# Kernel optimization log

Hardware: AMD Instinct MI355X
Metric: run time of the kernel (lower is better)

Reference implementation:

```python
import jax, jax.numpy as jnp
import numpy as np

B, MAXN, F, H, T, L = 32, 1024, 215, 256, 8, 3
N = B * MAXN            # 32768 global nodes
E = 524288              # total edges, global indices


def setup_inputs() -> dict:
    key = jax.random.key(0)
    ks = jax.random.split(key, 12)
    s = 0.05
    return {
        "node_features": jax.random.normal(ks[0], (B, MAXN, F), dtype=jnp.float32),
        "edge_index": jax.random.randint(ks[1], (2, E), 0, N, dtype=jnp.int32),
        "edge_type": jax.random.randint(ks[2], (E,), 0, T, dtype=jnp.int32),
        # input projection
        "Wp": jax.random.normal(ks[3], (H, F), dtype=jnp.float32) * s,
        "bp": jax.random.normal(ks[4], (H,), dtype=jnp.float32) * s,
        # per-layer, per-edge-type message linears
        "Wm": jax.random.normal(ks[5], (L, T, H, H), dtype=jnp.float32) * s,
        "bm": jax.random.normal(ks[6], (L, T, H), dtype=jnp.float32) * s,
        # per-layer GRUCell params (torch layout: [r|z|n] stacked, 3H rows)
        "Wih": jax.random.normal(ks[7], (L, 3 * H, H), dtype=jnp.float32) * s,
        "Whh": jax.random.normal(ks[8], (L, 3 * H, H), dtype=jnp.float32) * s,
        "bih": jax.random.normal(ks[9], (L, 3 * H), dtype=jnp.float32) * s,
        "bhh": jax.random.normal(ks[10], (L, 3 * H), dtype=jnp.float32) * s,
    }


def _gru_cell(x, h, Wih, Whh, bih, bhh):
    # torch.nn.GRUCell math
    gi = x @ Wih.T + bih            # (N, 3H)
    gh = h @ Whh.T + bhh            # (N, 3H)
    i_r, i_z, i_n = jnp.split(gi, 3, axis=-1)
    h_r, h_z, h_n = jnp.split(gh, 3, axis=-1)
    r = jax.nn.sigmoid(i_r + h_r)
    z = jax.nn.sigmoid(i_z + h_z)
    n = jnp.tanh(i_n + r * h_n)
    return (1.0 - z) * n + z * h


def reference(node_features, edge_index, edge_type, Wp, bp, Wm, bm, Wih, Whh, bih, bhh):
    # flatten batch of graphs into global node array, project to hidden
    h = node_features.reshape(-1, F) @ Wp.T + bp          # (N, H)
    src, dst = edge_index[0], edge_index[1]
    for l in range(L):
        # apply all T type-specific linears to every node once (equivalent to
        # the per-edge-type mask+gather+Linear loop), then gather per edge
        Ht = jnp.einsum('nd,ted->nte', h, Wm[l]) + bm[l]  # (N, T, H)
        msg = Ht[src, edge_type]                           # (E, H) gather
        m = jax.ops.segment_sum(msg, dst, num_segments=N)  # scatter-add (N, H)
        h = _gru_cell(m, h, Wih[l], Whh[l], bih[l], bhh[l])
        # dropout is identity in eval mode
    # readout: full graphs -> sum each graph's node block
    return h.reshape(B, MAXN, H).sum(axis=1)               # (B, H)
```

## Files before the change

### kernel.cpp

```cpp
#include <hip/hip_runtime.h>

#define N_NODES 32768
#define E_EDGES 524288
#define F_IN    215
#define H_DIM   256
#define T_TYPES 8
#define L_LAYERS 3
#define B_GRAPHS 32
#define MAXN_   1024
#define NT_BINS (N_NODES * T_TYPES)

typedef float  f32x4  __attribute__((ext_vector_type(4)));
typedef __bf16 bf16x8 __attribute__((ext_vector_type(8)));

__device__ __forceinline__ unsigned short f2bf(float f) {
  union { float f; unsigned u; } v; v.f = f;
  unsigned r = v.u + 0x7fffu + ((v.u >> 16) & 1u);
  return (unsigned short)(r >> 16);
}
__device__ __forceinline__ float bf2f(unsigned short h) {
  union { unsigned u; float f; } v; v.u = ((unsigned)h) << 16;
  return v.f;
}
__device__ __forceinline__ float bflo(unsigned u) { union { unsigned x; float f; } v; v.x = u << 16; return v.f; }
__device__ __forceinline__ float bfhi(unsigned u) { union { unsigned x; float f; } v; v.x = u & 0xffff0000u; return v.f; }

typedef const __attribute__((address_space(1))) unsigned int* gas_ptr;
typedef __attribute__((address_space(3))) unsigned int* las_ptr;
__device__ __forceinline__ void gload_lds16(const unsigned short* g, unsigned short* l) {
  __builtin_amdgcn_global_load_lds((gas_ptr)g, (las_ptr)l, 16, 0, 0);
}

__device__ __forceinline__ void acc16(float* a, const uint4 v, const uint4 w) {
  a[0]  += bflo(v.x); a[1]  += bfhi(v.x);
  a[2]  += bflo(v.y); a[3]  += bfhi(v.y);
  a[4]  += bflo(v.z); a[5]  += bfhi(v.z);
  a[6]  += bflo(v.w); a[7]  += bfhi(v.w);
  a[8]  += bflo(w.x); a[9]  += bfhi(w.x);
  a[10] += bflo(w.y); a[11] += bfhi(w.y);
  a[12] += bflo(w.z); a[13] += bfhi(w.z);
  a[14] += bflo(w.w); a[15] += bfhi(w.w);
}

static constexpr size_t OFF_BIG     = 0;
static constexpr size_t REL_CURSOR  = 1048576;
static constexpr size_t REL_BSUM    = 2097152;
static constexpr size_t REL_WPPAD   = 33554432;
static constexpr size_t REL_HALT    = 50331648;
static constexpr size_t REL_OFFS    = 100663296;
static constexpr size_t REL_SORTED  = 104857600;
static constexpr size_t OFF_H_B     = 134217728;
static constexpr size_t OFF_M_B     = 150994944;
static constexpr size_t OFF_WMB     = 167772160;
static constexpr size_t OFF_WIH     = 170917888;
static constexpr size_t OFF_WHH     = 172097536;
static constexpr size_t WS_REQUIRED = 173277184;

__global__ void hist_kernel(const int* __restrict__ dst, const int* __restrict__ et,
                            int* __restrict__ cnt) {
  int e = blockIdx.x * 256 + threadIdx.x;
  atomicAdd(&cnt[dst[e] * T_TYPES + et[e]], 1);
}

__global__ __launch_bounds__(1024) void scan1(const int* __restrict__ cnt,
                                              int* __restrict__ offs,
                                              int* __restrict__ bsum) {
  __shared__ int wsum[16];
  const int t = threadIdx.x, lane = t & 63, wid = t >> 6;
  const int idx = blockIdx.x * 1024 + t;
  const int v = cnt[idx];
  int x = v;
  #pragma unroll
  for (int off = 1; off < 64; off <<= 1) {
    int u = __shfl_up(x, off, 64);
    if (lane >= off) x += u;
  }
  if (lane == 63) wsum[wid] = x;
  __syncthreads();
  int wbase = 0;
  for (int i = 0; i < wid; ++i) wbase += wsum[i];
  offs[idx] = wbase + x - v;
  if (t == 1023) bsum[blockIdx.x] = wbase + x;
}

__global__ __launch_bounds__(256) void scan2(int* __restrict__ bsum) {
  __shared__ int wsum[4];
  const int t = threadIdx.x, lane = t & 63, wid = t >> 6;
  const int v = bsum[t];
  int x = v;
  #pragma unroll
  for (int off = 1; off < 64; off <<= 1) {
    int u = __shfl_up(x, off, 64);
    if (lane >= off) x += u;
  }
  if (lane == 63) wsum[wid] = x;
  __syncthreads();
  int wbase = 0;
  for (int i = 0; i < wid; ++i) wbase += wsum[i];
  __syncthreads();
  bsum[t] = wbase + x - v;
}

__global__ __launch_bounds__(1024) void scan3(int* __restrict__ offs,
                                              const int* __restrict__ bsum,
                                              int* __restrict__ cursor) {
  const int idx = blockIdx.x * 1024 + threadIdx.x;
  const int o = offs[idx] + bsum[blockIdx.x];
  offs[idx] = o;
  cursor[idx] = o;
  if (idx == 0) offs[NT_BINS] = E_EDGES;
}

__global__ void reorder_kernel(const int* __restrict__ src, const int* __restrict__ dst,
                               const int* __restrict__ et, int* __restrict__ cursor,
                               unsigned short* __restrict__ sorted) {
  int e = blockIdx.x * 256 + threadIdx.x;
  int key = dst[e] * T_TYPES + et[e];
  int p = atomicAdd(&cursor[key], 1);
  sorted[p] = (unsigned short)src[e];
}

__global__ void cvt_weights(const float* __restrict__ a, const float* __restrict__ b,
                            const float* __restrict__ c,
                            unsigned short* __restrict__ oa, unsigned short* __restrict__ ob,
                            unsigned short* __restrict__ oc,
                            int na, int nb, int nc) {
  int i = blockIdx.x * 256 + threadIdx.x;
  if (i < na) { oa[i] = f2bf(a[i]); return; }
  int j = i - na;
  if (j < nb) { ob[j] = f2bf(b[j]); return; }
  int k = j - nb;
  if (k < nc) oc[k] = f2bf(c[k]);
}

__global__ void pad_cvt(const float* __restrict__ in, unsigned short* __restrict__ out,
                        int rows, int cin) {
  int i = blockIdx.x * 256 + threadIdx.x;
  if (i >= rows * 256) return;
  int r = i >> 8, c = i & 255;
  out[i] = (c < cin) ? f2bf(in[(size_t)r * cin + c]) : (unsigned short)0;
}

__global__ __launch_bounds__(256, 2) void gemm_bt(
    const unsigned short* __restrict__ A,
    const unsigned short* __restrict__ W,
    const float* __restrict__ bias,
    unsigned short* __restrict__ C,
    int M, int K) {
  __shared__ unsigned short As[128 * 32];
  __shared__ unsigned short Bs[128 * 32];
  const int tid = threadIdx.x;
  const int lane = tid & 63;
  const int wv = tid >> 6;
  const int lrow = lane & 15;
  const int lquad = lane >> 4;
  const int bm0 = blockIdx.x * 128;
  const int bn0 = blockIdx.y * 128;
  const int srow = wv * 16 + (lane >> 2);
  const int scol = (lane & 3) * 8;

  f32x4 acc[2][8] = {};

  for (int kt = 0; kt < K; kt += 32) {
    #pragma unroll
    for (int i = 0; i < 2; ++i) {
      const int row = srow + i * 64;
      gload_lds16(A + (size_t)(bm0 + row) * K + kt + scol, &As[row * 32 + scol]);
      gload_lds16(W + (size_t)(bn0 + row) * K + kt + scol, &Bs[row * 32 + scol]);
    }
    __syncthreads();
    bf16x8 af[2], bfr[8];
    #pragma unroll
    for (int mt = 0; mt < 2; ++mt)
      af[mt] = *(const bf16x8*)(&As[(wv * 32 + mt * 16 + lrow) * 32 + lquad * 8]);
    #pragma unroll
    for (int nt = 0; nt < 8; ++nt)
      bfr[nt] = *(const bf16x8*)(&Bs[(nt * 16 + lrow) * 32 + lquad * 8]);
    #pragma unroll
    for (int mt = 0; mt < 2; ++mt)
      #pragma unroll
      for (int nt = 0; nt < 8; ++nt)
        acc[mt][nt] = __builtin_amdgcn_mfma_f32_16x16x32_bf16(af[mt], bfr[nt], acc[mt][nt], 0, 0, 0);
    __syncthreads();
  }

  #pragma unroll
  for (int mt = 0; mt < 2; ++mt) {
    #pragma unroll
    for (int r = 0; r < 4; ++r) {
      const int grow = bm0 + wv * 32 + mt * 16 + lquad * 4 + r;
      #pragma unroll
      for (int nt = 0; nt < 8; ++nt) {
        const int gcol = bn0 + nt * 16 + lrow;
        float v = acc[mt][nt][r] + (bias ? bias[gcol] : 0.f);
        C[(size_t)grow * M + gcol] = f2bf(v);
      }
    }
  }
}

__global__ __launch_bounds__(512, 4) void msg_gemm(
    const int* __restrict__ offs, const unsigned short* __restrict__ sorted,
    const unsigned short* __restrict__ hb, const unsigned short* __restrict__ Wt_l,
    const float* __restrict__ bm_l, unsigned short* __restrict__ m) {
  constexpr int CH = 2568;
  __shared__ unsigned short Ss[8 * CH];
  __shared__ unsigned short Bs[2][256 * 32];
  __shared__ unsigned short idxS[2048];
  __shared__ int offsS[516];
  const int tid = threadIdx.x;
  const int lane = tid & 63;
  const int wv = tid >> 6;
  const int lrow = lane & 15;
  const int lquad = lane >> 4;
  const int wrow = wv & 3;
  const int wcol = wv >> 2;
  const int bm0 = blockIdx.x * 64;
  const int gg = wv * 4 + lquad;
  const int brow = tid >> 2;
  const int bcol = (tid & 3) * 8;

  const int gseg0 = offs[bm0 * 8];
  const int gseg1 = offs[bm0 * 8 + 512];
  const int seg = gseg1 - gseg0;
  for (int i = tid; i < 513; i += 512) offsS[i] = offs[bm0 * 8 + i];
  const int segc = seg < 2048 ? seg : 2048;
  for (int i = tid; i < segc; i += 512) idxS[i] = sorted[gseg0 + i];
  const bool useLds = (seg <= 2048);
  const unsigned short* ip = useLds ? (const unsigned short*)idxS : (sorted + gseg0);
  __syncthreads();

  f32x4 acc[8] = {};
  int buf = 0;

  for (int t = 0; t < T_TYPES; ++t) {
    #pragma unroll
    for (int step = 0; step < 2; ++step) {
      const int dloc = gg + step * 32;
      const int beg = offsS[dloc * 8 + t] - gseg0;
      const int end = offsS[dloc * 8 + t + 1] - gseg0;
      float a[16];
      #pragma unroll
      for (int j = 0; j < 16; ++j) a[j] = 0.f;
      int e = beg;
      if (e + 2 <= end) {
        int s0 = ip[e], s1 = ip[e + 1];
        const unsigned short* h0 = hb + (size_t)s0 * H_DIM + lrow * 16;
        const unsigned short* h1 = hb + (size_t)s1 * H_DIM + lrow * 16;
        uint4 pv0 = *(const uint4*)h0, pw0 = *(const uint4*)(h0 + 8);
        uint4 pv1 = *(const uint4*)h1, pw1 = *(const uint4*)(h1 + 8);
        e += 2;
        for (; e + 2 <= end; e += 2) {
          const int n0 = ip[e], n1 = ip[e + 1];
          const unsigned short* g0 = hb + (size_t)n0 * H_DIM + lrow * 16;
          const unsigned short* g1 = hb + (size_t)n1 * H_DIM + lrow * 16;
          const uint4 nv0 = *(const uint4*)g0, nw0 = *(const uint4*)(g0 + 8);
          const uint4 nv1 = *(const uint4*)g1, nw1 = *(const uint4*)(g1 + 8);
          acc16(a, pv0, pw0);
          acc16(a, pv1, pw1);
          pv0 = nv0; pw0 = nw0; pv1 = nv1; pw1 = nw1;
        }
        acc16(a, pv0, pw0);
        acc16(a, pv1, pw1);
      }
      if (e < end) {
        const int s0 = ip[e];
        const unsigned short* h0 = hb + (size_t)s0 * H_DIM + lrow * 16;
        acc16(a, *(const uint4*)h0, *(const uint4*)(h0 + 8));
      }
      union { unsigned short us[16]; uint4 q[2]; } ob;
      #pragma unroll
      for (int j = 0; j < 16; ++j) ob.us[j] = f2bf(a[j]);
      uint4* p = (uint4*)&Ss[(lrow >> 1) * CH + dloc * 40 + (lrow & 1) * 16];
      p[0] = ob.q[0];
      p[1] = ob.q[1];
    }
    const unsigned short* Wt = Wt_l + (size_t)t * 65536;
    gload_lds16(Wt + (size_t)brow * 256 + bcol, &Bs[buf][brow * 32 + bcol]);
    gload_lds16(Wt + (size_t)(brow + 128) * 256 + bcol, &Bs[buf][(brow + 128) * 32 + bcol]);
    __syncthreads();
    for (int kc = 0; kc < 8; ++kc) {
      if (kc < 7) {
        gload_lds16(Wt + (size_t)brow * 256 + (kc + 1) * 32 + bcol,
                    &Bs[buf ^ 1][brow * 32 + bcol]);
        gload_lds16(Wt + (size_t)(brow + 128) * 256 + (kc + 1) * 32 + bcol,
                    &Bs[buf ^ 1][(brow + 128) * 32 + bcol]);
      }
      const bf16x8 af = *(const bf16x8*)(&Ss[kc * CH + (wrow * 16 + lrow) * 40 + lquad * 8]);
      #pragma unroll
      for (int nt = 0; nt < 8; ++nt) {
        const bf16x8 b = *(const bf16x8*)(&Bs[buf][((wcol * 8 + nt) * 16 + lrow) * 32 + lquad * 8]);
        acc[nt] = __builtin_amdgcn_mfma_f32_16x16x32_bf16(af, b, acc[nt], 0, 0, 0);
      }
      buf ^= 1;
      __syncthreads();
    }
  }

  float cnt[4][8];
  #pragma unroll
  for (int r = 0; r < 4; ++r) {
    const int dl = wrow * 16 + lquad * 4 + r;
    #pragma unroll
    for (int t = 0; t < 8; ++t)
      cnt[r][t] = (float)(offsS[dl * 8 + t + 1] - offsS[dl * 8 + t]);
  }
  #pragma unroll
  for (int nt = 0; nt < 8; ++nt) {
    const int gcol = wcol * 128 + nt * 16 + lrow;
    float bmv[8];
    #pragma unroll
    for (int t = 0; t < 8; ++t) bmv[t] = bm_l[t * H_DIM + gcol];
    #pragma unroll
    for (int r = 0; r < 4; ++r) {
      const int grow = bm0 + wrow * 16 + lquad * 4 + r;
      float v = acc[nt][r];
      #pragma unroll
      for (int t = 0; t < 8; ++t) v += cnt[r][t] * bmv[t];
      m[(size_t)grow * H_DIM + gcol] = f2bf(v);
    }
  }
}

__global__ __launch_bounds__(256, 3) void gru_fused(
    const unsigned short* __restrict__ mB,
    const unsigned short* __restrict__ hin,
    const unsigned short* __restrict__ wih_l,
    const unsigned short* __restrict__ whh_l,
    const float* __restrict__ bih_l,
    const float* __restrict__ bhh_l,
    unsigned short* __restrict__ hout) {
  __shared__ unsigned short Am[64 * 32];
  __shared__ unsigned short Ah[64 * 32];
  const int tid = threadIdx.x;
  const int lane = tid & 63;
  const int wv = tid >> 6;
  const int lrow = lane & 15;
  const int lquad = lane >> 4;
  const int n0 = blockIdx.x * 64;
  const int c0 = blockIdx.y * 64;
  const int arow = tid >> 2;
  const int scol = (tid & 3) * 8;

  f32x4 acc[6][4] = {};

  for (int kt = 0; kt < 256; kt += 32) {
    __syncthreads();
    gload_lds16(mB  + (size_t)(n0 + arow) * 256 + kt + scol, &Am[arow * 32 + scol]);
    gload_lds16(hin + (size_t)(n0 + arow) * 256 + kt + scol, &Ah[arow * 32 + scol]);
    __syncthreads();
    const int wr = c0 + wv * 16 + lrow;
    bf16x8 bfr[6];
    #pragma unroll
    for (int g = 0; g < 3; ++g) {
      bfr[g]     = *(const bf16x8*)(wih_l + (size_t)(g * 256 + wr) * 256 + kt + lquad * 8);
      bfr[g + 3] = *(const bf16x8*)(whh_l + (size_t)(g * 256 + wr) * 256 + kt + lquad * 8);
    }
    #pragma unroll
    for (int mt = 0; mt < 4; ++mt) {
      const bf16x8 am = *(const bf16x8*)(&Am[(mt * 16 + lrow) * 32 + lquad * 8]);
      const bf16x8 ah = *(const bf16x8*)(&Ah[(mt * 16 + lrow) * 32 + lquad * 8]);
      #pragma unroll
      for (int g = 0; g < 6; ++g)
        acc[g][mt] = __builtin_amdgcn_mfma_f32_16x16x32_bf16(g < 3 ? am : ah, bfr[g], acc[g][mt], 0, 0, 0);
    }
  }

  const int c = c0 + wv * 16 + lrow;
  const float b_ir = bih_l[c], b_iz = bih_l[256 + c], b_in = bih_l[512 + c];
  const float b_hr = bhh_l[c], b_hz = bhh_l[256 + c], b_hn = bhh_l[512 + c];
  #pragma unroll
  for (int mt = 0; mt < 4; ++mt) {
    #pragma unroll
    for (int r = 0; r < 4; ++r) {
      const int node = n0 + mt * 16 + lquad * 4 + r;
      const float i_r = acc[0][mt][r] + b_ir;
      const float i_z = acc[1][mt][r] + b_iz;
      const float i_n = acc[2][mt][r] + b_in;
      const float h_r = acc[3][mt][r] + b_hr;
      const float h_z = acc[4][mt][r] + b_hz;
      const float h_n = acc[5][mt][r] + b_hn;
      const float rr = 1.f / (1.f + __expf(-(i_r + h_r)));
      const float zz = 1.f / (1.f + __expf(-(i_z + h_z)));
      const float nn = tanhf(i_n + rr * h_n);
      const float hp = bf2f(hin[(size_t)node * 256 + c]);
      hout[(size_t)node * 256 + c] = f2bf((1.f - zz) * nn + zz * hp);
    }
  }
}

__global__ __launch_bounds__(256) void readout_partial(const unsigned short* __restrict__ hb,
                                                       float* __restrict__ part) {
  const int b = blockIdx.x >> 3;
  const int ch = blockIdx.x & 7;
  const int c = threadIdx.x;
  const unsigned short* base = hb + ((size_t)b * MAXN_ + ch * 128) * H_DIM + c;
  float s = 0.f;
  #pragma unroll 4
  for (int i = 0; i < 128; ++i) s += bf2f(base[(size_t)i * H_DIM]);
  part[(size_t)blockIdx.x * H_DIM + c] = s;
}

__global__ __launch_bounds__(256) void readout_final(const float* __restrict__ part,
                                                     float* __restrict__ out) {
  const int b = blockIdx.x;
  const int c = threadIdx.x;
  float s = 0.f;
  #pragma unroll
  for (int i = 0; i < 8; ++i) s += part[((size_t)b * 8 + i) * H_DIM + c];
  out[b * H_DIM + c] = s;
}

extern "C" void kernel_launch(void* const* d_in, const int* in_sizes, int n_in,
                              void* d_out, int out_size, void* d_ws, size_t ws_size,
                              hipStream_t stream) {
  if (ws_size < WS_REQUIRED) return;

  const float* X   = (const float*)d_in[0];
  const int*   ei  = (const int*)d_in[1];
  const int*   et  = (const int*)d_in[2];
  const float* Wp  = (const float*)d_in[3];
  const float* bp  = (const float*)d_in[4];
  const float* Wm  = (const float*)d_in[5];
  const float* bm  = (const float*)d_in[6];
  const float* Wih = (const float*)d_in[7];
  const float* Whh = (const float*)d_in[8];
  const float* bih = (const float*)d_in[9];
  const float* bhh = (const float*)d_in[10];
  float* out = (float*)d_out;
  char* ws = (char*)d_ws;

  int*            counts = (int*)(ws + OFF_BIG);
  int*            cursor = (int*)(ws + OFF_BIG + REL_CURSOR);
  int*            bsum   = (int*)(ws + OFF_BIG + REL_BSUM);
  unsigned short* xpad   = (unsigned short*)(ws + OFF_BIG);
  unsigned short* wppad  = (unsigned short*)(ws + OFF_BIG + REL_WPPAD);
  unsigned short* h_alt  = (unsigned short*)(ws + OFF_BIG + REL_HALT);
  float*          part   = (float*)(ws + OFF_BIG);
  int*            offs   = (int*)(ws + OFF_BIG + REL_OFFS);
  unsigned short* sorted = (unsigned short*)(ws + OFF_BIG + REL_SORTED);
  unsigned short* h_b    = (unsigned short*)(ws + OFF_H_B);
  unsigned short* m_b    = (unsigned short*)(ws + OFF_M_B);
  unsigned short* wmb    = (unsigned short*)(ws + OFF_WMB);
  unsigned short* wih_b  = (unsigned short*)(ws + OFF_WIH);
  unsigned short* whh_b  = (unsigned short*)(ws + OFF_WHH);

  const int* src = ei;
  const int* dst = ei + E_EDGES;

  hipMemsetAsync(counts, 0, NT_BINS * sizeof(int), stream);
  hist_kernel<<<E_EDGES / 256, 256, 0, stream>>>(dst, et, counts);
  scan1<<<NT_BINS / 1024, 1024, 0, stream>>>(counts, offs, bsum);
  scan2<<<1, 256, 0, stream>>>(bsum);
  scan3<<<NT_BINS / 1024, 1024, 0, stream>>>(offs, bsum, cursor);
  reorder_kernel<<<E_EDGES / 256, 256, 0, stream>>>(src, dst, et, cursor, sorted);

  pad_cvt<<<(N_NODES * 256) / 256, 256, 0, stream>>>(X, xpad, N_NODES, F_IN);
  pad_cvt<<<(256 * 256) / 256, 256, 0, stream>>>(Wp, wppad, 256, F_IN);
  {
    const int na = L_LAYERS * T_TYPES * H_DIM * H_DIM;
    const int nb = L_LAYERS * 3 * H_DIM * H_DIM;
    const int nc = nb;
    cvt_weights<<<(na + nb + nc + 255) / 256, 256, 0, stream>>>(
        Wm, Wih, Whh, wmb, wih_b, whh_b, na, nb, nc);
  }

  gemm_bt<<<dim3(N_NODES / 128, 2), 256, 0, stream>>>(xpad, wppad, bp, h_b, H_DIM, 256);

  for (int l = 0; l < L_LAYERS; ++l) {
    const unsigned short* wm_l  = wmb + (size_t)l * T_TYPES * H_DIM * H_DIM;
    const unsigned short* wih_l = wih_b + (size_t)l * 3 * H_DIM * H_DIM;
    const unsigned short* whh_l = whh_b + (size_t)l * 3 * H_DIM * H_DIM;
    const float* bm_l  = bm + (size_t)l * T_TYPES * H_DIM;
    const float* bih_l = bih + (size_t)l * 3 * H_DIM;
    const float* bhh_l = bhh + (size_t)l * 3 * H_DIM;

    unsigned short* h_cur = (l & 1) ? h_alt : h_b;
    unsigned short* h_nxt = (l & 1) ? h_b : h_alt;

    msg_gemm<<<N_NODES / 64, 512, 0, stream>>>(offs, sorted, h_cur, wm_l, bm_l, m_b);
    gru_fused<<<dim3(N_NODES / 64, 4), 256, 0, stream>>>(
        m_b, h_cur, wih_l, whh_l, bih_l, bhh_l, h_nxt);
  }

  readout_partial<<<B_GRAPHS * 8, 256, 0, stream>>>(h_alt, part);
  readout_final<<<B_GRAPHS, 256, 0, stream>>>(part, out);

  (void)in_sizes; (void)n_in; (void)out_size;
}
```

Measured before the change: 626.0 us.

## Double-buffer GEMM shared-memory staging and XOR-swizzle tiles to avoid bank conflicts

```diff
diff --git a/kernel.cpp b/kernel.cpp
--- a/kernel.cpp
+++ b/kernel.cpp
@@ -147,8 +147,8 @@
     const float* __restrict__ bias,
     unsigned short* __restrict__ C,
     int M, int K) {
-  __shared__ unsigned short As[128 * 32];
-  __shared__ unsigned short Bs[128 * 32];
+  __shared__ unsigned short As[2][128 * 32];
+  __shared__ unsigned short Bs[2][128 * 32];
   const int tid = threadIdx.x;
   const int lane = tid & 63;
   const int wv = tid >> 6;
@@ -157,25 +157,33 @@
   const int bm0 = blockIdx.x * 128;
   const int bn0 = blockIdx.y * 128;
   const int srow = wv * 16 + (lane >> 2);
-  const int scol = (lane & 3) * 8;
+  const int sslot = lane & 3;
+  const int scol = sslot * 8;
+  const int ssw = (sslot ^ ((lane >> 3) & 3)) * 8;
+  const int rsw = (lquad ^ ((lane >> 1) & 3)) * 8;
 
   f32x4 acc[2][8] = {};
 
-  for (int kt = 0; kt < K; kt += 32) {
-    #pragma unroll
-    for (int i = 0; i < 2; ++i) {
-      const int row = srow + i * 64;
-      gload_lds16(A + (size_t)(bm0 + row) * K + kt + scol, &As[row * 32 + scol]);
-      gload_lds16(W + (size_t)(bn0 + row) * K + kt + scol, &Bs[row * 32 + scol]);
-    }
-    __syncthreads();
+#define GBT_STAGE(b, kt)                                                              \
+  { _Pragma("unroll") for (int i = 0; i < 2; ++i) {                                   \
+      const int row = srow + i * 64;                                                  \
+      gload_lds16(A + (size_t)(bm0 + row) * K + (kt) + ssw, &As[b][row * 32 + scol]); \
+      gload_lds16(W + (size_t)(bn0 + row) * K + (kt) + ssw, &Bs[b][row * 32 + scol]); \
+    } }
+
+  GBT_STAGE(0, 0);
+  __syncthreads();
+  const int nk = K >> 5;
+  for (int ki = 0; ki < nk; ++ki) {
+    const int cur = ki & 1;
+    if (ki + 1 < nk) GBT_STAGE(cur ^ 1, (ki + 1) * 32);
     bf16x8 af[2], bfr[8];
     #pragma unroll
     for (int mt = 0; mt < 2; ++mt)
-      af[mt] = *(const bf16x8*)(&As[(wv * 32 + mt * 16 + lrow) * 32 + lquad * 8]);
+      af[mt] = *(const bf16x8*)(&As[cur][(wv * 32 + mt * 16 + lrow) * 32 + rsw]);
     #pragma unroll
     for (int nt = 0; nt < 8; ++nt)
-      bfr[nt] = *(const bf16x8*)(&Bs[(nt * 16 + lrow) * 32 + lquad * 8]);
+      bfr[nt] = *(const bf16x8*)(&Bs[cur][(nt * 16 + lrow) * 32 + rsw]);
     #pragma unroll
     for (int mt = 0; mt < 2; ++mt)
       #pragma unroll
@@ -183,6 +191,7 @@
         acc[mt][nt] = __builtin_amdgcn_mfma_f32_16x16x32_bf16(af[mt], bfr[nt], acc[mt][nt], 0, 0, 0);
     __syncthreads();
   }
+#undef GBT_STAGE
 
   #pragma unroll
   for (int mt = 0; mt < 2; ++mt) {
@@ -218,7 +227,10 @@
   const int bm0 = blockIdx.x * 64;
   const int gg = wv * 4 + lquad;
   const int brow = tid >> 2;
-  const int bcol = (tid & 3) * 8;
+  const int bslot = tid & 3;
+  const int bcol = bslot * 8;
+  const int bsw = (bslot ^ ((tid >> 3) & 3)) * 8;
+  const int rsw = (lquad ^ ((lane >> 1) & 3)) * 8;
 
   const int gseg0 = offs[bm0 * 8];
   const int gseg1 = offs[bm0 * 8 + 512];
@@ -276,20 +288,20 @@
       p[1] = ob.q[1];
     }
     const unsigned short* Wt = Wt_l + (size_t)t * 65536;
-    gload_lds16(Wt + (size_t)brow * 256 + bcol, &Bs[buf][brow * 32 + bcol]);
-    gload_lds16(Wt + (size_t)(brow + 128) * 256 + bcol, &Bs[buf][(brow + 128) * 32 + bcol]);
+    gload_lds16(Wt + (size_t)brow * 256 + bsw, &Bs[buf][brow * 32 + bcol]);
+    gload_lds16(Wt + (size_t)(brow + 128) * 256 + bsw, &Bs[buf][(brow + 128) * 32 + bcol]);
     __syncthreads();
     for (int kc = 0; kc < 8; ++kc) {
       if (kc < 7) {
-        gload_lds16(Wt + (size_t)brow * 256 + (kc + 1) * 32 + bcol,
+        gload_lds16(Wt + (size_t)brow * 256 + (kc + 1) * 32 + bsw,
                     &Bs[buf ^ 1][brow * 32 + bcol]);
-        gload_lds16(Wt + (size_t)(brow + 128) * 256 + (kc + 1) * 32 + bcol,
+        gload_lds16(Wt + (size_t)(brow + 128) * 256 + (kc + 1) * 32 + bsw,
                     &Bs[buf ^ 1][(brow + 128) * 32 + bcol]);
       }
       const bf16x8 af = *(const bf16x8*)(&Ss[kc * CH + (wrow * 16 + lrow) * 40 + lquad * 8]);
       #pragma unroll
       for (int nt = 0; nt < 8; ++nt) {
-        const bf16x8 b = *(const bf16x8*)(&Bs[buf][((wcol * 8 + nt) * 16 + lrow) * 32 + lquad * 8]);
+        const bf16x8 b = *(const bf16x8*)(&Bs[buf][((wcol * 8 + nt) * 16 + lrow) * 32 + rsw]);
         acc[nt] = __builtin_amdgcn_mfma_f32_16x16x32_bf16(af, b, acc[nt], 0, 0, 0);
       }
       buf ^= 1;
@@ -322,7 +334,7 @@
   }
 }
 
-__global__ __launch_bounds__(256, 3) void gru_fused(
+__global__ __launch_bounds__(256, 2) void gru_fused(
     const unsigned short* __restrict__ mB,
     const unsigned short* __restrict__ hin,
     const unsigned short* __restrict__ wih_l,
@@ -330,8 +342,8 @@
     const float* __restrict__ bih_l,
     const float* __restrict__ bhh_l,
     unsigned short* __restrict__ hout) {
-  __shared__ unsigned short Am[64 * 32];
-  __shared__ unsigned short Ah[64 * 32];
+  __shared__ unsigned short Am[2][64 * 32];
+  __shared__ unsigned short Ah[2][64 * 32];
   const int tid = threadIdx.x;
   const int lane = tid & 63;
   const int wv = tid >> 6;
@@ -340,31 +352,46 @@
   const int n0 = blockIdx.x * 64;
   const int c0 = blockIdx.y * 64;
   const int arow = tid >> 2;
-  const int scol = (tid & 3) * 8;
+  const int sslot = tid & 3;
+  const int ssw = (sslot ^ ((tid >> 3) & 3)) * 8;
+  const int rsw = (lquad ^ ((lane >> 1) & 3)) * 8;
+  const int wr = c0 + wv * 16 + lrow;
 
   f32x4 acc[6][4] = {};
-
-  for (int kt = 0; kt < 256; kt += 32) {
+  bf16x8 bfr[2][6];
+
+#define GRU_LOADB(bi, kt)                                                                      \
+  { _Pragma("unroll") for (int g = 0; g < 3; ++g) {                                            \
+      bfr[bi][g]     = *(const bf16x8*)(wih_l + (size_t)(g * 256 + wr) * 256 + (kt) + lquad * 8); \
+      bfr[bi][g + 3] = *(const bf16x8*)(whh_l + (size_t)(g * 256 + wr) * 256 + (kt) + lquad * 8); \
+    } }
+#define GRU_STAGE(b, kt)                                                                       \
+  { gload_lds16(mB  + (size_t)(n0 + arow) * 256 + (kt) + ssw, &Am[b][arow * 32 + sslot * 8]);  \
+    gload_lds16(hin + (size_t)(n0 + arow) * 256 + (kt) + ssw, &Ah[b][arow * 32 + sslot * 8]); }
+
+  GRU_LOADB(0, 0);
+  GRU_STAGE(0, 0);
+  __syncthreads();
+
+  #pragma unroll
+  for (int ki = 0; ki < 8; ++ki) {
+    const int cur = ki & 1;
+    if (ki < 7) {
+      GRU_LOADB(cur ^ 1, (ki + 1) * 32);
+      GRU_STAGE(cur ^ 1, (ki + 1) * 32);
+    }
+    #pragma unroll
+    for (int mt = 0; mt < 4; ++mt) {
+      const bf16x8 am = *(const bf16x8*)(&Am[cur][(mt * 16 + lrow) * 32 + rsw]);
+      const bf16x8 ah = *(const bf16x8*)(&Ah[cur][(mt * 16 + lrow) * 32 + rsw]);
+      #pragma unroll
+      for (int g = 0; g < 6; ++g)
+        acc[g][mt] = __builtin_amdgcn_mfma_f32_16x16x32_bf16(g < 3 ? am : ah, bfr[cur][g], acc[g][mt], 0, 0, 0);
+    }
     __syncthreads();
-    gload_lds16(mB  + (size_t)(n0 + arow) * 256 + kt + scol, &Am[arow * 32 + scol]);
-    gload_lds16(hin + (size_t)(n0 + arow) * 256 + kt + scol, &Ah[arow * 32 + scol]);
-    __syncthreads();
-    const int wr = c0 + wv * 16 + lrow;
-    bf16x8 bfr[6];
-    #pragma unroll
-    for (int g = 0; g < 3; ++g) {
-      bfr[g]     = *(const bf16x8*)(wih_l + (size_t)(g * 256 + wr) * 256 + kt + lquad * 8);
-      bfr[g + 3] = *(const bf16x8*)(whh_l + (size_t)(g * 256 + wr) * 256 + kt + lquad * 8);
-    }
-    #pragma unroll
-    for (int mt = 0; mt < 4; ++mt) {
-      const bf16x8 am = *(const bf16x8*)(&Am[(mt * 16 + lrow) * 32 + lquad * 8]);
-      const bf16x8 ah = *(const bf16x8*)(&Ah[(mt * 16 + lrow) * 32 + lquad * 8]);
-      #pragma unroll
-      for (int g = 0; g < 6; ++g)
-        acc[g][mt] = __builtin_amdgcn_mfma_f32_16x16x32_bf16(g < 3 ? am : ah, bfr[g], acc[g][mt], 0, 0, 0);
-    }
-  }
+  }
+#undef GRU_LOADB
+#undef GRU_STAGE
 
   const int c = c0 + wv * 16 + lrow;
   const float b_ir = bih_l[c], b_iz = bih_l[256 + c], b_in = bih_l[512 + c];
```

Result: slower. 641.1 us (+2.4%).
